# Kernel optimization log

Hardware: AMD Instinct MI355X
Metric: run time of the kernel (lower is better)

Reference implementation:

```python
import math
import jax, jax.numpy as jnp
import numpy as np

NA = 50000   # number of query nodes
NB = 50000   # number of key/value nodes
E = 800000   # number of edges
CA = 256
CB = 256
D = 256
H = 8
DH = D // H


def setup_inputs() -> dict:
    key = jax.random.key(0)
    ks = jax.random.split(key, 8)
    s = 1.0 / math.sqrt(CA)
    return {
        "Fa": jax.random.normal(ks[0], (NA, CA), dtype=jnp.float32),
        "Fb": jax.random.normal(ks[1], (NB, CB), dtype=jnp.float32),
        "a_idx": jax.random.randint(ks[2], (E,), 0, NA, dtype=jnp.int64)
        if jax.config.jax_enable_x64 else jax.random.randint(ks[2], (E,), 0, NA, dtype=jnp.int32),
        "b_idx": jax.random.randint(ks[3], (E,), 0, NB, dtype=jnp.int64)
        if jax.config.jax_enable_x64 else jax.random.randint(ks[3], (E,), 0, NB, dtype=jnp.int32),
        # torch nn.Linear weights: (out_features, in_features), y = x @ W.T
        "Wq": jax.random.normal(ks[4], (D, CA), dtype=jnp.float32) * s,
        "Wk": jax.random.normal(ks[5], (D, CB), dtype=jnp.float32) * s,
        "Wv": jax.random.normal(ks[6], (D, CB), dtype=jnp.float32) * s,
        "Wproj": jax.random.normal(ks[7], (CA, D), dtype=jnp.float32) * s,
    }


def _edge_attention(Q, K, V, Q_idx, K_idx, n_queries):
    # Q: (Na,H,dh)  K,V: (Nb,H,dh)  Q_idx,K_idx: (E,)
    scale = 1.0 / math.sqrt(Q.shape[-1])
    logits = jnp.sum(Q[Q_idx] * K[K_idx], axis=-1) * scale      # (E, H)
    # segmented softmax over edges sharing the same query (per head)
    seg_max = jax.ops.segment_max(logits, Q_idx, num_segments=n_queries)  # (Na, H)
    seg_max = jnp.where(jnp.isfinite(seg_max), seg_max, 0.0)
    ex = jnp.exp(logits - seg_max[Q_idx])                        # (E, H)
    seg_sum = jax.ops.segment_sum(ex, Q_idx, num_segments=n_queries)      # (Na, H)
    weights = ex / jnp.maximum(seg_sum[Q_idx], 1e-30)            # (E, H)
    # scatter-add weighted values
    out = jax.ops.segment_sum(weights[..., None] * V[K_idx], Q_idx,
                              num_segments=n_queries)            # (Na, H, dh)
    return out


def reference(Fa, Fb, a_idx, b_idx, Wq, Wk, Wv, Wproj):
    Na = Fa.shape[0]
    Q = (Fa @ Wq.T).reshape(Na, H, DH)
    K = (Fb @ Wk.T).reshape(-1, H, DH)
    V = (Fb @ Wv.T).reshape(-1, H, DH)
    out = _edge_attention(Q, K, V, a_idx, b_idx, Na)
    out = out.reshape(Na, H * DH)
    return Fa + out @ Wproj.T
```

## Files before the change

kernel.cpp:

```cpp
#include <hip/hip_runtime.h>

#define DM 256

typedef __attribute__((ext_vector_type(8))) short bf16x8;
typedef __attribute__((ext_vector_type(4))) float f32x4;
typedef __attribute__((ext_vector_type(4))) unsigned short us16x4;
typedef __attribute__((ext_vector_type(8))) unsigned short us16x8;
typedef unsigned short us16;

__device__ __forceinline__ unsigned short f2bf(float f) {
  unsigned int u = __float_as_uint(f);
  u += 0x7fffu + ((u >> 16) & 1u);
  return (unsigned short)(u >> 16);
}
__device__ __forceinline__ float bf2f(unsigned short s) {
  return __uint_as_float(((unsigned int)s) << 16);
}

__device__ __forceinline__ void gload16(const void* g, void* l) {
  __builtin_amdgcn_global_load_lds(
      (const __attribute__((address_space(1))) void*)g,
      (__attribute__((address_space(3))) void*)l, 16, 0, 0);
}

__global__ __launch_bounds__(512) void qkv_gemm(
    const float* __restrict__ Fa, const float* __restrict__ Fb,
    const us16* __restrict__ W_all, us16* __restrict__ Qbf,
    us16* __restrict__ KVbf, int NA, int NB)
{
  const int z = blockIdx.z;
  const float* A = (z == 0) ? Fa : Fb;
  const int Mreal = (z == 0) ? NA : NB;
  const int Mp = (Mreal + 127) & ~127;
  const us16* W = W_all + (size_t)z * 256 * 256;
  us16* Cb = (z == 0) ? Qbf : KVbf;
  const int ldc = (z == 0) ? 256 : 512;

  __shared__ us16 As[2][128 * 32];
  __shared__ us16 Bs[2][256 * 32];
  const int tid = threadIdx.x;
  const int w = tid >> 6, l = tid & 63;
  const int wr = w >> 2, wc = w & 3;
  const int rowBase = blockIdx.x * 128;
  if (rowBase >= Mp) return;
  const int ar = tid >> 2, ac = (tid & 3) * 8;
  const int grow0 = rowBase + ar;
  const bool aval = grow0 < Mreal;
  const float* Ap = A + (size_t)grow0 * 256 + ac;
  f32x4 acc[4][4] = {};

  {
    float4 x = make_float4(0.f, 0.f, 0.f, 0.f), y = x;
    if (aval) { x = *(const float4*)(Ap); y = *(const float4*)(Ap + 4); }
#pragma unroll
    for (int j = 0; j < 2; ++j) {
      const int r0 = (w * 2 + j) * 16;
      gload16(W + (size_t)(r0 + (l >> 2)) * 256 + (l & 3) * 8, &Bs[0][r0 * 32]);
    }
    bf16x8 av;
    av[0] = (short)f2bf(x.x); av[1] = (short)f2bf(x.y);
    av[2] = (short)f2bf(x.z); av[3] = (short)f2bf(x.w);
    av[4] = (short)f2bf(y.x); av[5] = (short)f2bf(y.y);
    av[6] = (short)f2bf(y.z); av[7] = (short)f2bf(y.w);
    *(bf16x8*)&As[0][ar * 32 + ac] = av;
  }
  __syncthreads();

  for (int t = 0; t < 8; ++t) {
    const int cur = t & 1, nxt = cur ^ 1;
    const bool pf = (t < 7);
    float4 x, y;
    if (pf) {
      const int k0 = (t + 1) * 32;
      x = make_float4(0.f, 0.f, 0.f, 0.f); y = x;
      if (aval) { x = *(const float4*)(Ap + k0); y = *(const float4*)(Ap + k0 + 4); }
#pragma unroll
      for (int j = 0; j < 2; ++j) {
        const int r0 = (w * 2 + j) * 16;
        gload16(W + (size_t)(r0 + (l >> 2)) * 256 + k0 + (l & 3) * 8,
                &Bs[nxt][r0 * 32]);
      }
    }
    bf16x8 af[4], bfr[4];
#pragma unroll
    for (int m = 0; m < 4; ++m)
      af[m] = *(const bf16x8*)&As[cur][(wr * 64 + m * 16 + (l & 15)) * 32 + (l >> 4) * 8];
#pragma unroll
    for (int n = 0; n < 4; ++n)
      bfr[n] = *(const bf16x8*)&Bs[cur][(wc * 64 + n * 16 + (l & 15)) * 32 + (l >> 4) * 8];
#pragma unroll
    for (int m = 0; m < 4; ++m)
#pragma unroll
      for (int n = 0; n < 4; ++n)
        acc[m][n] = __builtin_amdgcn_mfma_f32_16x16x32_bf16(af[m], bfr[n], acc[m][n], 0, 0, 0);
    if (pf) {
      bf16x8 av;
      av[0] = (short)f2bf(x.x); av[1] = (short)f2bf(x.y);
      av[2] = (short)f2bf(x.z); av[3] = (short)f2bf(x.w);
      av[4] = (short)f2bf(y.x); av[5] = (short)f2bf(y.y);
      av[6] = (short)f2bf(y.z); av[7] = (short)f2bf(y.w);
      *(bf16x8*)&As[nxt][ar * 32 + ac] = av;
    }
    __syncthreads();
  }

  const int er = (l >> 4) * 4;
  const int ec = l & 15;
  const int vofs = (z == 2) ? 4 : 0;
#pragma unroll
  for (int m = 0; m < 4; ++m)
#pragma unroll
    for (int n = 0; n < 4; ++n)
#pragma unroll
      for (int j = 0; j < 4; ++j) {
        const int grow = rowBase + wr * 64 + m * 16 + er + j;
        const int c = wc * 64 + n * 16 + ec;
        const int col = (z == 0) ? c : ((c >> 2) * 8 + (c & 3) + vofs);
        Cb[(size_t)grow * ldc + col] = f2bf(acc[m][n][j]);
      }
}

__global__ __launch_bounds__(512) void proj_gemm(
    const us16* __restrict__ A, const us16* __restrict__ W,
    float* __restrict__ Cf, const float* __restrict__ R, int Mreal)
{
  __shared__ us16 As[2][128 * 32];
  __shared__ us16 Bs[2][256 * 32];
  const int tid = threadIdx.x;
  const int w = tid >> 6, l = tid & 63;
  const int wr = w >> 2, wc = w & 3;
  const int rowBase = blockIdx.x * 128;
  f32x4 acc[4][4] = {};

  {
    const int r0 = w * 16;
    gload16(A + (size_t)(rowBase + r0 + (l >> 2)) * 256 + (l & 3) * 8,
            &As[0][r0 * 32]);
#pragma unroll
    for (int j = 0; j < 2; ++j) {
      const int rb = (w * 2 + j) * 16;
      gload16(W + (size_t)(rb + (l >> 2)) * 256 + (l & 3) * 8, &Bs[0][rb * 32]);
    }
  }
  __syncthreads();

  for (int t = 0; t < 8; ++t) {
    const int cur = t & 1, nxt = cur ^ 1;
    if (t < 7) {
      const int k0 = (t + 1) * 32;
      const int r0 = w * 16;
      gload16(A + (size_t)(rowBase + r0 + (l >> 2)) * 256 + k0 + (l & 3) * 8,
              &As[nxt][r0 * 32]);
#pragma unroll
      for (int j = 0; j < 2; ++j) {
        const int rb = (w * 2 + j) * 16;
        gload16(W + (size_t)(rb + (l >> 2)) * 256 + k0 + (l & 3) * 8,
                &Bs[nxt][rb * 32]);
      }
    }
    bf16x8 af[4], bfr[4];
#pragma unroll
    for (int m = 0; m < 4; ++m)
      af[m] = *(const bf16x8*)&As[cur][(wr * 64 + m * 16 + (l & 15)) * 32 + (l >> 4) * 8];
#pragma unroll
    for (int n = 0; n < 4; ++n)
      bfr[n] = *(const bf16x8*)&Bs[cur][(wc * 64 + n * 16 + (l & 15)) * 32 + (l >> 4) * 8];
#pragma unroll
    for (int m = 0; m < 4; ++m)
#pragma unroll
      for (int n = 0; n < 4; ++n)
        acc[m][n] = __builtin_amdgcn_mfma_f32_16x16x32_bf16(af[m], bfr[n], acc[m][n], 0, 0, 0);
    __syncthreads();
  }

  const int er = (l >> 4) * 4;
  const int ec = l & 15;
#pragma unroll
  for (int m = 0; m < 4; ++m)
#pragma unroll
    for (int n = 0; n < 4; ++n)
#pragma unroll
      for (int j = 0; j < 4; ++j) {
        const int grow = rowBase + wr * 64 + m * 16 + er + j;
        if (grow < Mreal) {
          const size_t off = (size_t)grow * 256 + wc * 64 + n * 16 + ec;
          Cf[off] = acc[m][n][j] + R[off];
        }
      }
}

__global__ void cvt_weights(const float* __restrict__ Wq, const float* __restrict__ Wk,
                            const float* __restrict__ Wv, const float* __restrict__ Wp,
                            us16* __restrict__ out)
{
  const int g = blockIdx.x * 256 + threadIdx.x;
  const size_t e = (size_t)g * 8;
  const int sel = (int)(e >> 16);
  const float* src = (sel == 0) ? Wq : (sel == 1) ? Wk : (sel == 2) ? Wv : Wp;
  const size_t loc = e & 65535;
  const float4 x = *(const float4*)(src + loc);
  const float4 y = *(const float4*)(src + loc + 4);
  bf16x8 o;
  o[0] = (short)f2bf(x.x); o[1] = (short)f2bf(x.y);
  o[2] = (short)f2bf(x.z); o[3] = (short)f2bf(x.w);
  o[4] = (short)f2bf(y.x); o[5] = (short)f2bf(y.y);
  o[6] = (short)f2bf(y.z); o[7] = (short)f2bf(y.w);
  *(bf16x8*)(out + e) = o;
}

__global__ void hist_kernel(const int* __restrict__ a_idx, int* __restrict__ counts, int E)
{
  const int e = blockIdx.x * 256 + threadIdx.x;
  if (e < E) atomicAdd(&counts[a_idx[e]], 1);
}

__global__ __launch_bounds__(256) void scan_offs(const int* __restrict__ counts,
    int* __restrict__ offs, int* __restrict__ cursor, int* __restrict__ total, int n)
{
  __shared__ int buf[256];
  __shared__ int sbase;
  const int t = threadIdx.x;
  const int i = blockIdx.x * 256 + t;
  const int v = (i < n) ? counts[i] : 0;
  buf[t] = v;
  __syncthreads();
#pragma unroll
  for (int off = 1; off < 256; off <<= 1) {
    const int x = (t >= off) ? buf[t - off] : 0;
    __syncthreads();
    buf[t] += x;
    __syncthreads();
  }
  const int incl = buf[t];
  if (t == 255) sbase = atomicAdd(total, incl);
  __syncthreads();
  if (i < n) {
    const int excl = sbase + incl - v;
    offs[i] = excl;
    cursor[i] = excl;
  }
}

__global__ void scatter_kernel(const int* __restrict__ a_idx, const int* __restrict__ b_idx,
    int* __restrict__ cursor, int* __restrict__ bel, int E)
{
  const int e = blockIdx.x * 256 + threadIdx.x;
  if (e < E) bel[atomicAdd(&cursor[a_idx[e]], 1)] = b_idx[e];
}

#define ATTN_STEP(S, J)                                        \
  if ((J) < cnt) {                                             \
    float p = q0 * bf2f(S[0]);                                 \
    p = fmaf(q1, bf2f(S[1]), p);                               \
    p = fmaf(q2, bf2f(S[2]), p);                               \
    p = fmaf(q3, bf2f(S[3]), p);                               \
    p += __shfl_xor(p, 1, 64);                                 \
    p += __shfl_xor(p, 2, 64);                                 \
    p += __shfl_xor(p, 4, 64);                                 \
    const float ex = __expf(p * scale);                        \
    ssum += ex;                                                \
    acc0 = fmaf(ex, bf2f(S[4]), acc0);                         \
    acc1 = fmaf(ex, bf2f(S[5]), acc1);                         \
    acc2 = fmaf(ex, bf2f(S[6]), acc2);                         \
    acc3 = fmaf(ex, bf2f(S[7]), acc3);                         \
  }

#define ATTN_LOAD(S, IDX)                                      \
  S = *(const us16x8*)(KVb + (size_t)bel[start + (IDX)] * 512 + l * 8);

__global__ __launch_bounds__(256) void edge_attn(
    const us16* __restrict__ Qb, const us16* __restrict__ KVb,
    const int* __restrict__ offs, const int* __restrict__ counts,
    const int* __restrict__ bel, us16* __restrict__ outb, int NA)
{
  const int a = blockIdx.x * 4 + (threadIdx.x >> 6);
  if (a >= NA) return;
  const int l = threadIdx.x & 63;
  const float scale = 0.17677669529663687f;

  const us16x4 q4 = *(const us16x4*)(Qb + (size_t)a * 256 + l * 4);
  const float q0 = bf2f(q4[0]), q1 = bf2f(q4[1]), q2 = bf2f(q4[2]), q3 = bf2f(q4[3]);

  const int start = offs[a];
  const int cnt = counts[a];
  float acc0 = 0.f, acc1 = 0.f, acc2 = 0.f, acc3 = 0.f, ssum = 0.f;

  if (cnt > 0) {
    const int last = cnt - 1;
    us16x8 sa, sb, sc, sd;
    ATTN_LOAD(sa, 0)
    ATTN_LOAD(sb, min(1, last))
    ATTN_LOAD(sc, min(2, last))
    ATTN_LOAD(sd, min(3, last))
    for (int i = 0; i < cnt; i += 4) {
      us16x8 na, nb, nc, nd;
      ATTN_LOAD(na, min(i + 4, last))
      ATTN_LOAD(nb, min(i + 5, last))
      ATTN_LOAD(nc, min(i + 6, last))
      ATTN_LOAD(nd, min(i + 7, last))
      ATTN_STEP(sa, i + 0)
      ATTN_STEP(sb, i + 1)
      ATTN_STEP(sc, i + 2)
      ATTN_STEP(sd, i + 3)
      sa = na; sb = nb; sc = nc; sd = nd;
    }
  }

  const float inv = (cnt > 0) ? 1.f / ssum : 0.f;
  us16x4 o;
  o[0] = f2bf(acc0 * inv); o[1] = f2bf(acc1 * inv);
  o[2] = f2bf(acc2 * inv); o[3] = f2bf(acc3 * inv);
  *(us16x4*)(outb + (size_t)a * 256 + l * 4) = o;
}

extern "C" void kernel_launch(void* const* d_in, const int* in_sizes, int n_in,
                              void* d_out, int out_size, void* d_ws, size_t ws_size,
                              hipStream_t stream)
{
  const float* Fa    = (const float*)d_in[0];
  const float* Fb    = (const float*)d_in[1];
  const int*   a_idx = (const int*)d_in[2];
  const int*   b_idx = (const int*)d_in[3];
  const float* Wq    = (const float*)d_in[4];
  const float* Wk    = (const float*)d_in[5];
  const float* Wv    = (const float*)d_in[6];
  const float* Wproj = (const float*)d_in[7];
  float* out = (float*)d_out;

  const int NA = in_sizes[0] / DM;
  const int NB = in_sizes[1] / DM;
  const int E  = in_sizes[2];
  const int MAp = (NA + 127) & ~127;
  const int NBp = (NB + 127) & ~127;
  const int MXp = (MAp > NBp) ? MAp : NBp;

  us16* Qbf   = (us16*)d_ws;
  us16* KVbf  = Qbf   + (size_t)MAp * 256;
  us16* ATbf  = KVbf  + (size_t)NBp * 512;
  us16* W_all = ATbf  + (size_t)MAp * 256;
  int* total  = (int*)(W_all + 1024 * 256);
  int* counts = total + 1;
  int* offs   = counts + NA;
  int* cursor = offs + NA;
  int* bel    = cursor + NA;

  hipMemsetAsync(total, 0, (size_t)(NA + 1) * sizeof(int), stream);

  cvt_weights<<<128, 256, 0, stream>>>(Wq, Wk, Wv, Wproj, W_all);

  hist_kernel<<<(E + 255) / 256, 256, 0, stream>>>(a_idx, counts, E);
  scan_offs<<<(NA + 255) / 256, 256, 0, stream>>>(counts, offs, cursor, total, NA);
  scatter_kernel<<<(E + 255) / 256, 256, 0, stream>>>(a_idx, b_idx, cursor, bel, E);

  qkv_gemm<<<dim3(MXp / 128, 1, 3), 512, 0, stream>>>(Fa, Fb, W_all, Qbf, KVbf, NA, NB);

  edge_attn<<<(NA + 3) / 4, 256, 0, stream>>>(Qbf, KVbf, offs, counts, bel, ATbf, NA);

  proj_gemm<<<dim3(MAp / 128, 1), 512, 0, stream>>>(ATbf, W_all + 768 * 256, out, Fa, NA);
}
```

Measured before the change: 438.2 us.

## Split K/V layout, fold softmax scale into Q, process two queries per wave

The QKV GEMM now writes K and V as separate contiguous 256-wide halves, and it pre-multiplies Q by scale*log2(e) so the attention kernel can use exp2f without a separate multiply. The edge attention kernel assigns 32 lanes per query, so each wave handles two queries, with each lane covering 8 head dims via 16-byte K and V loads and a shorter shuffle reduction. This halves the number of waves and raises per-lane work and memory-level parallelism. In exchange, the two half-waves are bound to the maximum edge count of the pair, which adds divergence, and register pressure goes up.

```diff
diff --git a/kernel.cpp b/kernel.cpp
--- a/kernel.cpp
+++ b/kernel.cpp
@@ -1,6 +1,7 @@
 #include <hip/hip_runtime.h>
 
 #define DM 256
+#define QSCALE 0.25503403f
 
 typedef __attribute__((ext_vector_type(8))) short bf16x8;
 typedef __attribute__((ext_vector_type(4))) float f32x4;
@@ -35,6 +36,7 @@
   const us16* W = W_all + (size_t)z * 256 * 256;
   us16* Cb = (z == 0) ? Qbf : KVbf;
   const int ldc = (z == 0) ? 256 : 512;
+  const int colofs = (z == 2) ? 256 : 0;
 
   __shared__ us16 As[2][128 * 32];
   __shared__ us16 Bs[2][256 * 32];
@@ -106,7 +108,6 @@
 
   const int er = (l >> 4) * 4;
   const int ec = l & 15;
-  const int vofs = (z == 2) ? 4 : 0;
 #pragma unroll
   for (int m = 0; m < 4; ++m)
 #pragma unroll
@@ -115,8 +116,9 @@
       for (int j = 0; j < 4; ++j) {
         const int grow = rowBase + wr * 64 + m * 16 + er + j;
         const int c = wc * 64 + n * 16 + ec;
-        const int col = (z == 0) ? c : ((c >> 2) * 8 + (c & 3) + vofs);
-        Cb[(size_t)grow * ldc + col] = f2bf(acc[m][n][j]);
+        float v = acc[m][n][j];
+        if (z == 0) v *= QSCALE;
+        Cb[(size_t)grow * ldc + c + colofs] = f2bf(v);
       }
 }
 
@@ -248,69 +250,91 @@
   if (e < E) bel[atomicAdd(&cursor[a_idx[e]], 1)] = b_idx[e];
 }
 
-#define ATTN_STEP(S, J)                                        \
+#define ATTN_STEP(K, V, J)                                     \
   if ((J) < cnt) {                                             \
-    float p = q0 * bf2f(S[0]);                                 \
-    p = fmaf(q1, bf2f(S[1]), p);                               \
-    p = fmaf(q2, bf2f(S[2]), p);                               \
-    p = fmaf(q3, bf2f(S[3]), p);                               \
+    float p = q0 * bf2f(K[0]);                                 \
+    p = fmaf(q1, bf2f(K[1]), p);                               \
+    p = fmaf(q2, bf2f(K[2]), p);                               \
+    p = fmaf(q3, bf2f(K[3]), p);                               \
+    p = fmaf(q4, bf2f(K[4]), p);                               \
+    p = fmaf(q5, bf2f(K[5]), p);                               \
+    p = fmaf(q6, bf2f(K[6]), p);                               \
+    p = fmaf(q7, bf2f(K[7]), p);                               \
     p += __shfl_xor(p, 1, 64);                                 \
     p += __shfl_xor(p, 2, 64);                                 \
-    p += __shfl_xor(p, 4, 64);                                 \
-    const float ex = __expf(p * scale);                        \
+    const float ex = exp2f(p);                                 \
     ssum += ex;                                                \
-    acc0 = fmaf(ex, bf2f(S[4]), acc0);                         \
-    acc1 = fmaf(ex, bf2f(S[5]), acc1);                         \
-    acc2 = fmaf(ex, bf2f(S[6]), acc2);                         \
-    acc3 = fmaf(ex, bf2f(S[7]), acc3);                         \
-  }
-
-#define ATTN_LOAD(S, IDX)                                      \
-  S = *(const us16x8*)(KVb + (size_t)bel[start + (IDX)] * 512 + l * 8);
+    acc0 = fmaf(ex, bf2f(V[0]), acc0);                         \
+    acc1 = fmaf(ex, bf2f(V[1]), acc1);                         \
+    acc2 = fmaf(ex, bf2f(V[2]), acc2);                         \
+    acc3 = fmaf(ex, bf2f(V[3]), acc3);                         \
+    acc4 = fmaf(ex, bf2f(V[4]), acc4);                         \
+    acc5 = fmaf(ex, bf2f(V[5]), acc5);                         \
+    acc6 = fmaf(ex, bf2f(V[6]), acc6);                         \
+    acc7 = fmaf(ex, bf2f(V[7]), acc7);                         \
+  }
+
+#define ATTN_LOAD(K, V, IDX)                                   \
+  {                                                            \
+    const us16* kv = KVb + (size_t)bel[sstart + (IDX)] * 512 + kvo; \
+    K = *(const us16x8*)(kv);                                  \
+    V = *(const us16x8*)(kv + 256);                            \
+  }
 
 __global__ __launch_bounds__(256) void edge_attn(
     const us16* __restrict__ Qb, const us16* __restrict__ KVb,
     const int* __restrict__ offs, const int* __restrict__ counts,
     const int* __restrict__ bel, us16* __restrict__ outb, int NA)
 {
-  const int a = blockIdx.x * 4 + (threadIdx.x >> 6);
-  if (a >= NA) return;
-  const int l = threadIdx.x & 63;
-  const float scale = 0.17677669529663687f;
-
-  const us16x4 q4 = *(const us16x4*)(Qb + (size_t)a * 256 + l * 4);
-  const float q0 = bf2f(q4[0]), q1 = bf2f(q4[1]), q2 = bf2f(q4[2]), q3 = bf2f(q4[3]);
-
-  const int start = offs[a];
-  const int cnt = counts[a];
-  float acc0 = 0.f, acc1 = 0.f, acc2 = 0.f, acc3 = 0.f, ssum = 0.f;
-
-  if (cnt > 0) {
-    const int last = cnt - 1;
-    us16x8 sa, sb, sc, sd;
-    ATTN_LOAD(sa, 0)
-    ATTN_LOAD(sb, min(1, last))
-    ATTN_LOAD(sc, min(2, last))
-    ATTN_LOAD(sd, min(3, last))
-    for (int i = 0; i < cnt; i += 4) {
-      us16x8 na, nb, nc, nd;
-      ATTN_LOAD(na, min(i + 4, last))
-      ATTN_LOAD(nb, min(i + 5, last))
-      ATTN_LOAD(nc, min(i + 6, last))
-      ATTN_LOAD(nd, min(i + 7, last))
-      ATTN_STEP(sa, i + 0)
-      ATTN_STEP(sb, i + 1)
-      ATTN_STEP(sc, i + 2)
-      ATTN_STEP(sd, i + 3)
-      sa = na; sb = nb; sc = nc; sd = nd;
-    }
-  }
-
-  const float inv = (cnt > 0) ? 1.f / ssum : 0.f;
-  us16x4 o;
-  o[0] = f2bf(acc0 * inv); o[1] = f2bf(acc1 * inv);
-  o[2] = f2bf(acc2 * inv); o[3] = f2bf(acc3 * inv);
-  *(us16x4*)(outb + (size_t)a * 256 + l * 4) = o;
+  const int a = blockIdx.x * 8 + (threadIdx.x >> 5);
+  const int hd = threadIdx.x & 31;
+  const int kvo = hd * 8;
+  const bool valid = (a < NA);
+
+  const int aa = valid ? a : (NA - 1);
+  const us16x8 q8 = *(const us16x8*)(Qb + (size_t)aa * 256 + kvo);
+  const float q0 = bf2f(q8[0]), q1 = bf2f(q8[1]), q2 = bf2f(q8[2]), q3 = bf2f(q8[3]);
+  const float q4 = bf2f(q8[4]), q5 = bf2f(q8[5]), q6 = bf2f(q8[6]), q7 = bf2f(q8[7]);
+
+  const int cnt = valid ? counts[a] : 0;
+  const int sstart = (cnt > 0) ? offs[a] : 0;
+  const int last = (cnt > 0) ? cnt - 1 : 0;
+  const int mcnt = max(cnt, __shfl_xor(cnt, 32, 64));
+
+  float acc0 = 0.f, acc1 = 0.f, acc2 = 0.f, acc3 = 0.f;
+  float acc4 = 0.f, acc5 = 0.f, acc6 = 0.f, acc7 = 0.f;
+  float ssum = 0.f;
+
+  if (mcnt > 0) {
+    us16x8 ka, va, kb, vb, kc, vc, kd, vd;
+    ATTN_LOAD(ka, va, 0)
+    ATTN_LOAD(kb, vb, min(1, last))
+    ATTN_LOAD(kc, vc, min(2, last))
+    ATTN_LOAD(kd, vd, min(3, last))
+    for (int i = 0; i < mcnt; i += 4) {
+      us16x8 na, xa, nb, xb, nc, xc, nd, xd;
+      ATTN_LOAD(na, xa, min(i + 4, last))
+      ATTN_LOAD(nb, xb, min(i + 5, last))
+      ATTN_LOAD(nc, xc, min(i + 6, last))
+      ATTN_LOAD(nd, xd, min(i + 7, last))
+      ATTN_STEP(ka, va, i + 0)
+      ATTN_STEP(kb, vb, i + 1)
+      ATTN_STEP(kc, vc, i + 2)
+      ATTN_STEP(kd, vd, i + 3)
+      ka = na; va = xa; kb = nb; vb = xb;
+      kc = nc; vc = xc; kd = nd; vd = xd;
+    }
+  }
+
+  if (valid) {
+    const float inv = (cnt > 0) ? 1.f / ssum : 0.f;
+    us16x8 o;
+    o[0] = (short)f2bf(acc0 * inv); o[1] = (short)f2bf(acc1 * inv);
+    o[2] = (short)f2bf(acc2 * inv); o[3] = (short)f2bf(acc3 * inv);
+    o[4] = (short)f2bf(acc4 * inv); o[5] = (short)f2bf(acc5 * inv);
+    o[6] = (short)f2bf(acc6 * inv); o[7] = (short)f2bf(acc7 * inv);
+    *(us16x8*)(outb + (size_t)a * 256 + kvo) = o;
+  }
 }
 
 extern "C" void kernel_launch(void* const* d_in, const int* in_sizes, int n_in,
@@ -354,7 +378,7 @@
 
   qkv_gemm<<<dim3(MXp / 128, 1, 3), 512, 0, stream>>>(Fa, Fb, W_all, Qbf, KVbf, NA, NB);
 
-  edge_attn<<<(NA + 3) / 4, 256, 0, stream>>>(Qbf, KVbf, offs, counts, bel, ATbf, NA);
+  edge_attn<<<(NA + 7) / 8, 256, 0, stream>>>(Qbf, KVbf, offs, counts, bel, ATbf, NA);
 
   proj_gemm<<<dim3(MAp / 128, 1), 512, 0, stream>>>(ATbf, W_all + 768 * 256, out, Fa, NA);
 }
```

After: 439.5 us. Within noise of the previous version (+0.3%).
